# Optimization experiments

Hardware: AMD Instinct MI355X
Metric: run time of the kernel (lower is better)

## Reference

```python
import jax, jax.numpy as jnp
import numpy as np

N = 50000          # nodes per node type
F = 256            # input feature dim
C = 256            # hidden_channels
H, D = 8, 32       # heads, head_dim (C = H*D)
E = 200000         # edges per edge type
OUT = 16           # out_channels
SRC = (0, 1, 0)    # edge type -> source node-type index (user,item)
DST = (1, 0, 0)    # edge type -> destination node-type index
LABELED = 1        # labeled_class = 'item'


def setup_inputs() -> dict:
    key = jax.random.key(0)
    ks = jax.random.split(key, 24)
    s = 0.06  # ~1/sqrt(256) init scale
    inp = {
        'x': jax.random.normal(ks[0], (2, N, F), jnp.float32),
        'edge_index': jax.random.randint(ks[1], (3, 2, E), 0, N, jnp.int64),
        'lin_w': jax.random.normal(ks[2], (2, F, C), jnp.float32) * s,
        'lin_b': jnp.zeros((2, C), jnp.float32),
        'k_w': jax.random.normal(ks[3], (2, C, C), jnp.float32) * s,
        'k_b': jnp.zeros((2, C), jnp.float32),
        'q_w': jax.random.normal(ks[4], (2, C, C), jnp.float32) * s,
        'q_b': jnp.zeros((2, C), jnp.float32),
        'v_w': jax.random.normal(ks[5], (2, C, C), jnp.float32) * s,
        'v_b': jnp.zeros((2, C), jnp.float32),
        'a_w': jax.random.normal(ks[6], (2, C, C), jnp.float32) * s,
        'a_b': jnp.zeros((2, C), jnp.float32),
        'skip': jnp.ones((2,), jnp.float32),
        'a_rel': jax.random.normal(ks[7], (3, H, D, D), jnp.float32) * (1.0 / np.sqrt(D)),
        'm_rel': jax.random.normal(ks[8], (3, H, D, D), jnp.float32) * (1.0 / np.sqrt(D)),
        'p_rel': jnp.ones((3, H), jnp.float32),
        'out_w': jax.random.normal(ks[9], (C, OUT), jnp.float32) * s,
        'out_b': jnp.zeros((OUT,), jnp.float32),
    }
    return inp


def _segment_softmax(alpha, idx, n):
    # alpha: [E, H], idx: [E] destination node ids
    amax = jax.ops.segment_max(alpha, idx, num_segments=n)
    amax = jnp.where(jnp.isfinite(amax), amax, 0.0)
    ex = jnp.exp(alpha - amax[idx])
    den = jax.ops.segment_sum(ex, idx, num_segments=n)
    return ex / (den[idx] + 1e-16)


def reference(x, edge_index, lin_w, lin_b, k_w, k_b, q_w, q_b, v_w, v_b,
              a_w, a_b, skip, a_rel, m_rel, p_rel, out_w, out_b):
    # per-node-type input Linear + ReLU
    h = jax.nn.relu(jnp.einsum('tnf,tfc->tnc', x, lin_w) + lin_b[:, None, :])

    def proj(w, b):
        return (jnp.einsum('tnc,tce->tne', h, w) + b[:, None, :]).reshape(2, N, H, D)

    k = proj(k_w, k_b)
    q = proj(q_w, q_b)
    v = proj(v_w, v_b)

    agg = jnp.zeros((2, N, H, D), h.dtype)
    for t in range(3):  # fixed small loop over edge types
        s, d = SRC[t], DST[t]
        src_idx, dst_idx = edge_index[t, 0], edge_index[t, 1]
        # relation-specific transforms of source keys / values
        k_rel = jnp.einsum('nhd,hde->nhe', k[s], a_rel[t])
        v_rel = jnp.einsum('nhd,hde->nhe', v[s], m_rel[t])
        # per-edge attention logits [E, H]
        alpha = (q[d][dst_idx] * k_rel[src_idx]).sum(-1) * p_rel[t] / (D ** 0.5)
        alpha = _segment_softmax(alpha, dst_idx, N)
        msg = v_rel[src_idx] * alpha[..., None]          # [E, H, D]
        agg = agg.at[d].add(jax.ops.segment_sum(msg, dst_idx, num_segments=N))

    o = agg.reshape(2, N, C)
    o = jnp.einsum('tnc,tce->tne', jax.nn.gelu(o, approximate=False), a_w) + a_b[:, None, :]
    beta = jax.nn.sigmoid(skip)[:, None, None]
    o = beta * o + (1.0 - beta) * h                      # skip connection (in == out dims)

    return o[LABELED] @ out_w + out_b                    # logits for labeled_class='item'
```

## Files before the change

kernel.cpp:

```cpp
#include <hip/hip_runtime.h>
#include <hip/hip_bf16.h>

using u16 = unsigned short;
using u32 = unsigned int;

#define NNODES 50000
#define NEDGE  200000
#define DEGCAP 64
#define NT     3125

__device__ __forceinline__ float blo2f(u32 u) { u32 v = u << 16; float f; __builtin_memcpy(&f, &v, 4); return f; }
__device__ __forceinline__ float bhi2f(u32 u) { u32 v = u & 0xffff0000u; float f; __builtin_memcpy(&f, &v, 4); return f; }
__device__ __forceinline__ u16 f2b(float f) {
  __hip_bfloat16 h = __float2bfloat16(f);
  u16 r; __builtin_memcpy(&r, &h, 2); return r;
}
__device__ __forceinline__ float gelu_exact(float x) {
  return 0.5f * x * (1.f + erff(x * 0.70710678118654752f));
}

__device__ __forceinline__ void gload16(const void* gp, void* lp) {
  __builtin_amdgcn_global_load_lds(
      (__attribute__((address_space(1))) u32*)(const_cast<void*>(gp)),
      (__attribute__((address_space(3))) u32*)lp, 16, 0, 0);
}

#define WAIT_VM(N) asm volatile("s_waitcnt vmcnt(" #N ")" ::: "memory")

typedef __bf16 bh8 __attribute__((ext_vector_type(8)));
typedef float f32x4 __attribute__((ext_vector_type(4)));

struct GArg { const u16* A; const u16* B; const float* bias; u16* C; };

__device__ __forceinline__ void stage_blk_bf16(const u16* At, u16* buf, int wave, int lane) {
#pragma unroll
  for (int i = 0; i < 2; ++i) {
    const int row = wave * 4 + i * 2 + (lane >> 5);
    const int c   = (lane & 31) ^ (row & 7);
    gload16(At + (size_t)row * 256 + c * 8, buf + wave * 1024 + i * 512 + lane * 8);
  }
}

__device__ __forceinline__ void stage_blk_f32(const float* At, float* buf, int wave, int lane) {
#pragma unroll
  for (int i = 0; i < 4; ++i) {
    const int row = wave * 4 + i;
    const int c   = lane ^ (row & 7);
    gload16(At + (size_t)row * 256 + c * 4, buf + row * 256 + lane * 4);
  }
}

template <int MODE, bool F32A>
__launch_bounds__(256, 2)
__global__ void gemm_v10(GArg g0, GArg g1, GArg g2)
{
  GArg ga = (blockIdx.z == 0) ? g0 : ((blockIdx.z == 1) ? g1 : g2);
  const int tid  = threadIdx.x;
  const int lane = tid & 63;
  const int wave = tid >> 6;
  const int lr = lane & 15;
  const int lq = lane >> 4;
  const int colbase = wave * 64;

  constexpr int TW = F32A ? 8192 : 4096;
  __shared__ alignas(16) u16 lds[3][TW];
  __shared__ alignas(16) u16 pat[4][1152];
  u16* wl = &pat[wave][0];

  bh8 B[4][8];
#pragma unroll
  for (int s = 0; s < 4; ++s) {
    const u16* bp = ga.B + (size_t)(colbase + s * 16 + lr) * 256 + lq * 8;
#pragma unroll
    for (int ks = 0; ks < 8; ++ks) B[s][ks] = *(const bh8*)(bp + ks * 32);
  }
  float bias[4];
#pragma unroll
  for (int s = 0; s < 4; ++s) bias[s] = ga.bias[colbase + s * 16 + lr];

  int foffL[8], foffH[8];
#pragma unroll
  for (int ks = 0; ks < 8; ++ks) {
    if (F32A) {
      foffL[ks] = lr * 256 + (((ks * 8 + lq * 2)     ^ (lr & 7)) << 2);
      foffH[ks] = lr * 256 + (((ks * 8 + lq * 2 + 1) ^ (lr & 7)) << 2);
    } else {
      foffL[ks] = lr * 256 + (((ks * 4 + lq) ^ (lr & 7)) * 8);
    }
  }

  const int t0 = blockIdx.x;
  const int ts = gridDim.x;

  if (F32A) stage_blk_f32((const float*)ga.A + (size_t)t0 * 4096, (float*)&lds[0][0], wave, lane);
  else      stage_blk_bf16(ga.A + (size_t)t0 * 4096, &lds[0][0], wave, lane);
  if (t0 + ts < NT) {
    if (F32A) stage_blk_f32((const float*)ga.A + (size_t)(t0 + ts) * 4096, (float*)&lds[1][0], wave, lane);
    else      stage_blk_bf16(ga.A + (size_t)(t0 + ts) * 4096, &lds[1][0], wave, lane);
  }

  int it = 0, rb = 0;
  for (int t = t0; t < NT; t += ts, ++it) {
    const bool p1 = (t + ts < NT), p2 = (t + 2 * ts < NT);
    if (p2) {
      const int rn = (rb + 2 >= 3) ? rb - 1 : rb + 2;
      if (F32A) stage_blk_f32((const float*)ga.A + (size_t)(t + 2 * ts) * 4096, (float*)&lds[rn][0], wave, lane);
      else      stage_blk_bf16(ga.A + (size_t)(t + 2 * ts) * 4096, &lds[rn][0], wave, lane);
    }
    if (!p1)            { WAIT_VM(0); }
    else if (!p2)       { if (F32A) { WAIT_VM(6); }  else { WAIT_VM(4); } }
    else if (it >= 2)   { if (F32A) { WAIT_VM(12); } else { WAIT_VM(8); } }
    else                { if (F32A) { WAIT_VM(8); }  else { WAIT_VM(4); } }
    __builtin_amdgcn_s_barrier();

    bh8 ab[8];
    if (F32A) {
      const float* fbuf = (const float*)&lds[rb][0];
#pragma unroll
      for (int ks = 0; ks < 8; ++ks) {
        const f32x4 lo = *(const f32x4*)(fbuf + foffL[ks]);
        const f32x4 hi = *(const f32x4*)(fbuf + foffH[ks]);
#pragma unroll
        for (int j = 0; j < 4; ++j) { ab[ks][j] = (__bf16)lo[j]; ab[ks][j + 4] = (__bf16)hi[j]; }
      }
    } else {
      const u16* buf = &lds[rb][0];
#pragma unroll
      for (int ks = 0; ks < 8; ++ks) ab[ks] = *(const bh8*)(buf + foffL[ks]);
    }

    f32x4 acc[4];
#pragma unroll
    for (int s = 0; s < 4; ++s) acc[s] = (f32x4){0.f, 0.f, 0.f, 0.f};
#pragma unroll
    for (int ks = 0; ks < 8; ++ks) {
#pragma unroll
      for (int s = 0; s < 4; ++s)
        acc[s] = __builtin_amdgcn_mfma_f32_16x16x32_bf16(ab[ks], B[s][ks], acc[s], 0, 0, 0);
    }

#pragma unroll
    for (int s = 0; s < 4; ++s) {
#pragma unroll
      for (int r = 0; r < 4; ++r) {
        float v = acc[s][r] + bias[s];
        if (MODE == 0) v = fmaxf(v, 0.f);
        wl[(lq * 4 + r) * 72 + s * 16 + lr] = f2b(v);
      }
    }
#pragma unroll
    for (int j = 0; j < 2; ++j) {
      const int row = (lane >> 3) + j * 8;
      const int seg = lane & 7;
      const uint4 pv = *(const uint4*)(wl + row * 72 + seg * 8);
      *(uint4*)(ga.C + ((size_t)t * 16 + row) * 256 + colbase + seg * 8) = pv;
    }
    __builtin_amdgcn_s_barrier();
    rb = (rb + 1 == 3) ? 0 : rb + 1;
  }
}

__global__ void prep_w_k(const float* __restrict__ lin_w, const float* __restrict__ q_w,
                         const float* __restrict__ a_w, const float* __restrict__ k_w,
                         const float* __restrict__ v_w, const float* __restrict__ k_b,
                         const float* __restrict__ v_b, const float* __restrict__ a_rel,
                         const float* __restrict__ m_rel, const float* __restrict__ out_w,
                         const float* __restrict__ a_b, const float* __restrict__ out_b,
                         const float* __restrict__ skipv,
                         u16* __restrict__ lin0T, u16* __restrict__ lin1T,
                         u16* __restrict__ qT,
                         u16* __restrict__ kfT, u16* __restrict__ vfT,
                         u16* __restrict__ WcT, float* __restrict__ bfin,
                         float* __restrict__ bkf, float* __restrict__ bvf,
                         int* __restrict__ cnt)
{
  const int tid = blockIdx.x * 256 + threadIdx.x;
  const int nn = tid >> 8, kk = tid & 255;
  switch (blockIdx.y) {
    case 0: lin0T[tid] = f2b(lin_w[kk * 256 + nn]); break;
    case 1: lin1T[tid] = f2b(lin_w[65536 + kk * 256 + nn]); break;
    case 2: qT[tid] = f2b(q_w[65536 + kk * 256 + nn]); break;
    case 3: {
      const int h = nn >> 5, e = nn & 31;
      float s = 0.f;
      for (int d = 0; d < 32; ++d) s += k_w[kk * 256 + h * 32 + d] * a_rel[(h * 32 + d) * 32 + e];
      kfT[tid] = f2b(s);
      if (kk == 0) {
        float sb = 0.f;
        for (int d = 0; d < 32; ++d) sb += k_b[h * 32 + d] * a_rel[(h * 32 + d) * 32 + e];
        bkf[nn] = sb;
      }
      break;
    }
    case 4: {
      const int h = nn >> 5, e = nn & 31;
      float s = 0.f;
      for (int d = 0; d < 32; ++d) s += v_w[kk * 256 + h * 32 + d] * m_rel[(h * 32 + d) * 32 + e];
      vfT[tid] = f2b(s);
      if (kk == 0) {
        float sb = 0.f;
        for (int d = 0; d < 32; ++d) sb += v_b[h * 32 + d] * m_rel[(h * 32 + d) * 32 + e];
        bvf[nn] = sb;
      }
      break;
    }
    case 5: {
      const float beta = 1.f / (1.f + __expf(-skipv[1]));
      if (tid < 8192) {
        const int j = tid & 15;
        const int k = tid >> 4;
        float s;
        if (k < 256) {
          float acc = 0.f;
          for (int d = 0; d < 256; ++d)
            acc += a_w[65536 + k * 256 + d] * out_w[d * 16 + j];
          s = beta * acc;
        } else {
          s = (1.f - beta) * out_w[(k - 256) * 16 + j];
        }
        WcT[j * 512 + k] = f2b(s);
      }
      if (tid < 16) {
        float acc = 0.f;
        for (int c = 0; c < 256; ++c) acc += a_b[256 + c] * out_w[c * 16 + tid];
        bfin[tid] = beta * acc + out_b[tid];
      }
      break;
    }
    default:
      if (tid < NNODES) cnt[tid] = 0;
      break;
  }
}

__global__ void scatter_k(const int* __restrict__ ei, int* __restrict__ cnt, int* __restrict__ srcl) {
  const int e = blockIdx.x * 256 + threadIdx.x;
  if (e >= NEDGE) return;
  const int src = ei[e];
  const int dst = ei[NEDGE + e];
  if ((unsigned)dst >= NNODES || (unsigned)src >= NNODES) return;
  const int pos = atomicAdd(&cnt[dst], 1);
  if (pos < DEGCAP) srcl[(size_t)dst * DEGCAP + pos] = src;
}

__global__ void edge_agg_k(const u16* __restrict__ qb, const u16* __restrict__ krel,
                           const u16* __restrict__ vrel, const int* __restrict__ cnt,
                           const int* __restrict__ srcl, const float* __restrict__ prel,
                           u16* __restrict__ g)
{
  const int node = (blockIdx.x * blockDim.x + threadIdx.x) >> 6;
  if (node >= NNODES) return;
  const int lane = threadIdx.x & 63;
  const int hh = lane >> 3;
  const int off = hh * 32 + (lane & 7) * 4;
  const float scale = prel[hh] * 0.17677669529663687f;
  const uint2 qv = *(const uint2*)(qb + (size_t)node * 256 + off);
  const float q0 = blo2f(qv.x) * scale, q1 = bhi2f(qv.x) * scale;
  const float q2 = blo2f(qv.y) * scale, q3 = bhi2f(qv.y) * scale;
  int dg = cnt[node]; if (dg > DEGCAP) dg = DEGCAP;
  const int mysrc = srcl[(size_t)node * DEGCAP + lane];

  float den = 0.f, a0 = 0.f, a1 = 0.f, a2 = 0.f, a3 = 0.f;
  uint2 kv = {0, 0}, vv = {0, 0};
  if (dg > 0) {
    const int s0 = __shfl(mysrc, 0);
    kv = *(const uint2*)(krel + (size_t)s0 * 256 + off);
    vv = *(const uint2*)(vrel + (size_t)s0 * 256 + off);
  }
  for (int i = 0; i < dg; ++i) {
    uint2 kn = kv, vn = vv;
    if (i + 1 < dg) {
      const int sn = __shfl(mysrc, i + 1);
      kn = *(const uint2*)(krel + (size_t)sn * 256 + off);
      vn = *(const uint2*)(vrel + (size_t)sn * 256 + off);
    }
    float p = q0 * blo2f(kv.x) + q1 * bhi2f(kv.x) + q2 * blo2f(kv.y) + q3 * bhi2f(kv.y);
    p += __shfl_xor(p, 1);
    p += __shfl_xor(p, 2);
    p += __shfl_xor(p, 4);
    const float ex = __expf(p);
    den += ex;
    a0 += ex * blo2f(vv.x); a1 += ex * bhi2f(vv.x);
    a2 += ex * blo2f(vv.y); a3 += ex * bhi2f(vv.y);
    kv = kn; vv = vn;
  }
  float r0 = 0.f, r1 = 0.f, r2 = 0.f, r3 = 0.f;
  if (dg > 0) {
    const float inv = 1.f / den;
    r0 = gelu_exact(a0 * inv); r1 = gelu_exact(a1 * inv);
    r2 = gelu_exact(a2 * inv); r3 = gelu_exact(a3 * inv);
  }
  uint2 gv;
  gv.x = (u32)f2b(r0) | ((u32)f2b(r1) << 16);
  gv.y = (u32)f2b(r2) | ((u32)f2b(r3) << 16);
  *(uint2*)(g + (size_t)node * 256 + off) = gv;
}

__launch_bounds__(256, 3)
__global__ void final_v10(const u16* __restrict__ g, const u16* __restrict__ h1,
                          const u16* __restrict__ WcT, const float* __restrict__ bfin,
                          float* __restrict__ out)
{
  const int tid = threadIdx.x;
  const int lane = tid & 63;
  const int wave = tid >> 6;
  const int lr = lane & 15;
  const int lq = lane >> 4;

  __shared__ alignas(16) u16 lds[3][8192];
  __shared__ float red[4][256];

  bh8 B[4];
  {
    const u16* bp = WcT + (size_t)lr * 512 + wave * 128 + lq * 8;
#pragma unroll
    for (int ks = 0; ks < 4; ++ks) B[ks] = *(const bh8*)(bp + ks * 32);
  }
  const float bv = bfin[tid & 15];

  int foff[4];
#pragma unroll
  for (int ks = 0; ks < 4; ++ks)
    foff[ks] = wave * 2048 + lr * 128 + (((ks * 4 + lq) ^ (lr & 7)) * 8);

  const u16* srcq = (wave < 2) ? g + wave * 128 : h1 + (wave - 2) * 128;

  const int t0 = blockIdx.x;
  const int ts = gridDim.x;

#define FSTAGE(T, RB)                                                          \
  {                                                                            \
    _Pragma("unroll")                                                          \
    for (int i = 0; i < 4; ++i) {                                              \
      const int row = i * 4 + (lane >> 4);                                     \
      const int c   = (lane & 15) ^ (row & 7);                                 \
      gload16(srcq + (size_t)(T) * 4096 + row * 256 + c * 8,                   \
              &lds[RB][wave * 2048 + i * 512 + lane * 8]);                     \
    }                                                                          \
  }

  FSTAGE(t0, 0);
  if (t0 + ts < NT) FSTAGE(t0 + ts, 1);

  int it = 0, rb = 0;
  for (int t = t0; t < NT; t += ts, ++it) {
    const bool p1 = (t + ts < NT), p2 = (t + 2 * ts < NT);
    if (p2) {
      const int rn = (rb + 2 >= 3) ? rb - 1 : rb + 2;
      FSTAGE(t + 2 * ts, rn);
    }
    if (!p1)          { WAIT_VM(0); }
    else if (!p2)     { WAIT_VM(4); }
    else if (it >= 2) { WAIT_VM(10); }
    else              { WAIT_VM(8); }
    __builtin_amdgcn_s_barrier();

    f32x4 acc = {0.f, 0.f, 0.f, 0.f};
    const u16* buf = &lds[rb][0];
#pragma unroll
    for (int ks = 0; ks < 4; ++ks)
      acc = __builtin_amdgcn_mfma_f32_16x16x32_bf16(*(const bh8*)(buf + foff[ks]), B[ks], acc, 0, 0, 0);

#pragma unroll
    for (int r = 0; r < 4; ++r) red[wave][(lq * 4 + r) * 16 + lr] = acc[r];
    asm volatile("s_waitcnt lgkmcnt(0)" ::: "memory");
    __builtin_amdgcn_s_barrier();

    const float s = red[0][tid] + red[1][tid] + red[2][tid] + red[3][tid] + bv;
    out[(size_t)t * 256 + tid] = s;
    __builtin_amdgcn_s_barrier();
    rb = (rb + 1 == 3) ? 0 : rb + 1;
  }
#undef FSTAGE
}

extern "C" void kernel_launch(void* const* d_in, const int* in_sizes, int n_in,
                              void* d_out, int out_size, void* d_ws, size_t ws_size,
                              hipStream_t stream)
{
  const float* x     = (const float*)d_in[0];
  const int*   ei    = (const int*)d_in[1];
  const float* lin_w = (const float*)d_in[2];
  const float* lin_b = (const float*)d_in[3];
  const float* k_w   = (const float*)d_in[4];
  const float* k_b   = (const float*)d_in[5];
  const float* q_w   = (const float*)d_in[6];
  const float* q_b   = (const float*)d_in[7];
  const float* v_w   = (const float*)d_in[8];
  const float* v_b   = (const float*)d_in[9];
  const float* a_w   = (const float*)d_in[10];
  const float* a_b   = (const float*)d_in[11];
  const float* skipv = (const float*)d_in[12];
  const float* a_rel = (const float*)d_in[13];
  const float* m_rel = (const float*)d_in[14];
  const float* p_rel = (const float*)d_in[15];
  const float* out_w = (const float*)d_in[16];
  const float* out_b = (const float*)d_in[17];
  char* ws = (char*)d_ws;

  u16*  h0    = (u16*)(ws + 0);
  u16*  h1    = (u16*)(ws + 25600000);
  u16*  qb    = (u16*)(ws + 51200000);
  u16*  krel  = (u16*)(ws + 76800000);
  u16*  vrel  = (u16*)(ws + 102400000);
  u16*  gbuf  = (u16*)(ws + 128000000);
  char* W     = ws + 153600000;
  u16*  lin0T = (u16*)(W + 0);
  u16*  lin1T = (u16*)(W + 131072);
  u16*  qT    = (u16*)(W + 2 * 131072);
  u16*  kfT   = (u16*)(W + 3 * 131072);
  u16*  vfT   = (u16*)(W + 4 * 131072);
  u16*  WcT   = (u16*)(W + 5 * 131072);
  float* bfin = (float*)(W + 5 * 131072 + 16384);
  float* bkf  = (float*)(W + 5 * 131072 + 17408);
  float* bvf  = (float*)(W + 5 * 131072 + 18432);
  int*  cnt   = (int*)(W + 5 * 131072 + 19456);
  int*  srcl  = (int*)(W + 5 * 131072 + 19456 + 200000);

  prep_w_k<<<dim3(256, 7), 256, 0, stream>>>(lin_w, q_w, a_w, k_w, v_w, k_b, v_b,
                                             a_rel, m_rel, out_w, a_b, out_b, skipv,
                                             lin0T, lin1T, qT, kfT, vfT, WcT, bfin,
                                             bkf, bvf, cnt);
  scatter_k<<<(NEDGE + 255) / 256, 256, 0, stream>>>(ei, cnt, srcl);

  {
    GArg a0{(const u16*)x, lin0T, lin_b, h0};
    GArg a1{(const u16*)(x + (size_t)NNODES * 256), lin1T, lin_b + 256, h1};
    gemm_v10<0, true><<<dim3(256, 1, 2), 256, 0, stream>>>(a0, a1, a0);
  }
  {
    GArg a0{h1, qT, q_b + 256, qb};
    GArg a1{h0, kfT, bkf, krel};
    GArg a2{h0, vfT, bvf, vrel};
    gemm_v10<1, false><<<dim3(170, 1, 3), 256, 0, stream>>>(a0, a1, a2);
  }
  edge_agg_k<<<12500, 256, 0, stream>>>(qb, krel, vrel, cnt, srcl, p_rel, gbuf);
  final_v10<<<768, 256, 0, stream>>>(gbuf, h1, WcT, bfin, (float*)d_out);
}
```

Baseline: 322.4 us.

## Split GEMM columns across blocks and use register-staged double buffering

```diff
diff --git a/kernel.cpp b/kernel.cpp
--- a/kernel.cpp
+++ b/kernel.cpp
@@ -32,27 +32,9 @@
 
 struct GArg { const u16* A; const u16* B; const float* bias; u16* C; };
 
-__device__ __forceinline__ void stage_blk_bf16(const u16* At, u16* buf, int wave, int lane) {
-#pragma unroll
-  for (int i = 0; i < 2; ++i) {
-    const int row = wave * 4 + i * 2 + (lane >> 5);
-    const int c   = (lane & 31) ^ (row & 7);
-    gload16(At + (size_t)row * 256 + c * 8, buf + wave * 1024 + i * 512 + lane * 8);
-  }
-}
-
-__device__ __forceinline__ void stage_blk_f32(const float* At, float* buf, int wave, int lane) {
-#pragma unroll
-  for (int i = 0; i < 4; ++i) {
-    const int row = wave * 4 + i;
-    const int c   = lane ^ (row & 7);
-    gload16(At + (size_t)row * 256 + c * 4, buf + row * 256 + lane * 4);
-  }
-}
-
 template <int MODE, bool F32A>
-__launch_bounds__(256, 2)
-__global__ void gemm_v10(GArg g0, GArg g1, GArg g2)
+__launch_bounds__(256, 3)
+__global__ void gemm_v14(GArg g0, GArg g1, GArg g2)
 {
   GArg ga = (blockIdx.z == 0) ? g0 : ((blockIdx.z == 1) ? g1 : g2);
   const int tid  = threadIdx.x;
@@ -60,23 +42,23 @@
   const int wave = tid >> 6;
   const int lr = lane & 15;
   const int lq = lane >> 4;
-  const int colbase = wave * 64;
+  const int colbase = blockIdx.y * 128 + wave * 32;
 
   constexpr int TW = F32A ? 8192 : 4096;
-  __shared__ alignas(16) u16 lds[3][TW];
-  __shared__ alignas(16) u16 pat[4][1152];
+  __shared__ alignas(16) u16 lds[2][TW];
+  __shared__ alignas(16) u16 pat[4][640];
   u16* wl = &pat[wave][0];
 
-  bh8 B[4][8];
-#pragma unroll
-  for (int s = 0; s < 4; ++s) {
+  bh8 B[2][8];
+#pragma unroll
+  for (int s = 0; s < 2; ++s) {
     const u16* bp = ga.B + (size_t)(colbase + s * 16 + lr) * 256 + lq * 8;
 #pragma unroll
     for (int ks = 0; ks < 8; ++ks) B[s][ks] = *(const bh8*)(bp + ks * 32);
   }
-  float bias[4];
-#pragma unroll
-  for (int s = 0; s < 4; ++s) bias[s] = ga.bias[colbase + s * 16 + lr];
+  float bias[2];
+#pragma unroll
+  for (int s = 0; s < 2; ++s) bias[s] = ga.bias[colbase + s * 16 + lr];
 
   int foffL[8], foffH[8];
 #pragma unroll
@@ -92,30 +74,54 @@
   const int t0 = blockIdx.x;
   const int ts = gridDim.x;
 
-  if (F32A) stage_blk_f32((const float*)ga.A + (size_t)t0 * 4096, (float*)&lds[0][0], wave, lane);
-  else      stage_blk_bf16(ga.A + (size_t)t0 * 4096, &lds[0][0], wave, lane);
-  if (t0 + ts < NT) {
-    if (F32A) stage_blk_f32((const float*)ga.A + (size_t)(t0 + ts) * 4096, (float*)&lds[1][0], wave, lane);
-    else      stage_blk_bf16(ga.A + (size_t)(t0 + ts) * 4096, &lds[1][0], wave, lane);
-  }
-
-  int it = 0, rb = 0;
-  for (int t = t0; t < NT; t += ts, ++it) {
-    const bool p1 = (t + ts < NT), p2 = (t + 2 * ts < NT);
-    if (p2) {
-      const int rn = (rb + 2 >= 3) ? rb - 1 : rb + 2;
-      if (F32A) stage_blk_f32((const float*)ga.A + (size_t)(t + 2 * ts) * 4096, (float*)&lds[rn][0], wave, lane);
-      else      stage_blk_bf16(ga.A + (size_t)(t + 2 * ts) * 4096, &lds[rn][0], wave, lane);
-    }
-    if (!p1)            { WAIT_VM(0); }
-    else if (!p2)       { if (F32A) { WAIT_VM(6); }  else { WAIT_VM(4); } }
-    else if (it >= 2)   { if (F32A) { WAIT_VM(12); } else { WAIT_VM(8); } }
-    else                { if (F32A) { WAIT_VM(8); }  else { WAIT_VM(4); } }
-    __builtin_amdgcn_s_barrier();
+  f32x4 rf[4];
+  uint4  rb2[2];
+
+#define LOADR(T)                                                               \
+  if (F32A) {                                                                  \
+    const float* ap = (const float*)ga.A + ((size_t)(T) * 16 + wave * 4) * 256 \
+                      + lane * 4;                                              \
+    _Pragma("unroll")                                                          \
+    for (int i = 0; i < 4; ++i) rf[i] = *(const f32x4*)(ap + i * 256);         \
+  } else {                                                                     \
+    _Pragma("unroll")                                                          \
+    for (int i = 0; i < 2; ++i) {                                              \
+      const int row = wave * 4 + i * 2 + (lane >> 5);                          \
+      rb2[i] = *(const uint4*)(ga.A + ((size_t)(T) * 16 + row) * 256           \
+                               + (lane & 31) * 8);                             \
+    }                                                                          \
+  }
+
+#define WRITER(P)                                                              \
+  if (F32A) {                                                                  \
+    float* bp = (float*)&lds[P][0];                                            \
+    _Pragma("unroll")                                                          \
+    for (int i = 0; i < 4; ++i) {                                              \
+      const int row = wave * 4 + i;                                            \
+      *(f32x4*)(bp + row * 256 + ((lane ^ (row & 7)) << 2)) = rf[i];           \
+    }                                                                          \
+  } else {                                                                     \
+    _Pragma("unroll")                                                          \
+    for (int i = 0; i < 2; ++i) {                                              \
+      const int row = wave * 4 + i * 2 + (lane >> 5);                          \
+      *(uint4*)(&lds[P][row * 256 + (((lane & 31) ^ (row & 7)) * 8)]) = rb2[i];\
+    }                                                                          \
+  }
+
+  LOADR(t0);
+  WAIT_VM(0);
+  WRITER(0);
+  asm volatile("s_waitcnt lgkmcnt(0)" ::: "memory");
+  __builtin_amdgcn_s_barrier();
+
+  int p = 0;
+  for (int t = t0; t < NT; t += ts) {
+    const bool pn = (t + ts < NT);
+    if (pn) LOADR(t + ts);
 
     bh8 ab[8];
     if (F32A) {
-      const float* fbuf = (const float*)&lds[rb][0];
+      const float* fbuf = (const float*)&lds[p][0];
 #pragma unroll
       for (int ks = 0; ks < 8; ++ks) {
         const f32x4 lo = *(const f32x4*)(fbuf + foffL[ks]);
@@ -124,40 +130,46 @@
         for (int j = 0; j < 4; ++j) { ab[ks][j] = (__bf16)lo[j]; ab[ks][j + 4] = (__bf16)hi[j]; }
       }
     } else {
-      const u16* buf = &lds[rb][0];
+      const u16* buf = &lds[p][0];
 #pragma unroll
       for (int ks = 0; ks < 8; ++ks) ab[ks] = *(const bh8*)(buf + foffL[ks]);
     }
 
-    f32x4 acc[4];
-#pragma unroll
-    for (int s = 0; s < 4; ++s) acc[s] = (f32x4){0.f, 0.f, 0.f, 0.f};
+    f32x4 acc[2];
+#pragma unroll
+    for (int s = 0; s < 2; ++s) acc[s] = (f32x4){0.f, 0.f, 0.f, 0.f};
 #pragma unroll
     for (int ks = 0; ks < 8; ++ks) {
 #pragma unroll
-      for (int s = 0; s < 4; ++s)
+      for (int s = 0; s < 2; ++s)
         acc[s] = __builtin_amdgcn_mfma_f32_16x16x32_bf16(ab[ks], B[s][ks], acc[s], 0, 0, 0);
     }
 
 #pragma unroll
-    for (int s = 0; s < 4; ++s) {
+    for (int s = 0; s < 2; ++s) {
 #pragma unroll
       for (int r = 0; r < 4; ++r) {
         float v = acc[s][r] + bias[s];
         if (MODE == 0) v = fmaxf(v, 0.f);
-        wl[(lq * 4 + r) * 72 + s * 16 + lr] = f2b(v);
-      }
-    }
-#pragma unroll
-    for (int j = 0; j < 2; ++j) {
-      const int row = (lane >> 3) + j * 8;
-      const int seg = lane & 7;
-      const uint4 pv = *(const uint4*)(wl + row * 72 + seg * 8);
+        wl[(lq * 4 + r) * 40 + s * 16 + lr] = f2b(v);
+      }
+    }
+    {
+      const int row = lane >> 2, seg = lane & 3;
+      const uint4 pv = *(const uint4*)(wl + row * 40 + seg * 8);
       *(uint4*)(ga.C + ((size_t)t * 16 + row) * 256 + colbase + seg * 8) = pv;
     }
+
+    if (pn) {
+      WAIT_VM(1);
+      WRITER(p ^ 1);
+    }
+    asm volatile("s_waitcnt lgkmcnt(0)" ::: "memory");
     __builtin_amdgcn_s_barrier();
-    rb = (rb + 1 == 3) ? 0 : rb + 1;
-  }
+    p ^= 1;
+  }
+#undef LOADR
+#undef WRITER
 }
 
 __global__ void prep_w_k(const float* __restrict__ lin_w, const float* __restrict__ q_w,
@@ -426,13 +438,13 @@
   {
     GArg a0{(const u16*)x, lin0T, lin_b, h0};
     GArg a1{(const u16*)(x + (size_t)NNODES * 256), lin1T, lin_b + 256, h1};
-    gemm_v10<0, true><<<dim3(256, 1, 2), 256, 0, stream>>>(a0, a1, a0);
+    gemm_v14<0, true><<<dim3(192, 2, 2), 256, 0, stream>>>(a0, a1, a0);
   }
   {
     GArg a0{h1, qT, q_b + 256, qb};
     GArg a1{h0, kfT, bkf, krel};
     GArg a2{h0, vfT, bvf, vrel};
-    gemm_v10<1, false><<<dim3(170, 1, 3), 256, 0, stream>>>(a0, a1, a2);
+    gemm_v14<1, false><<<dim3(128, 2, 3), 256, 0, stream>>>(a0, a1, a2);
   }
   edge_agg_k<<<12500, 256, 0, stream>>>(qb, krel, vrel, cnt, srcl, p_rel, gbuf);
   final_v10<<<768, 256, 0, stream>>>(gbuf, h1, WcT, bfin, (float*)d_out);
```

Result: slower. 341.7 us (+6.0%).

## Fuse edge aggregation with final output projection into one persistent kernel

Applied to the files above, without the earlier changes.

```diff
diff --git a/kernel.cpp b/kernel.cpp
--- a/kernel.cpp
+++ b/kernel.cpp
@@ -14,6 +14,9 @@
 __device__ __forceinline__ u16 f2b(float f) {
   __hip_bfloat16 h = __float2bfloat16(f);
   u16 r; __builtin_memcpy(&r, &h, 2); return r;
+}
+__device__ __forceinline__ u32 pack2(float a, float b) {
+  return (u32)f2b(a) | ((u32)f2b(b) << 16);
 }
 __device__ __forceinline__ float gelu_exact(float x) {
   return 0.5f * x * (1.f + erff(x * 0.70710678118654752f));
@@ -170,7 +173,7 @@
                          u16* __restrict__ lin0T, u16* __restrict__ lin1T,
                          u16* __restrict__ qT,
                          u16* __restrict__ kfT, u16* __restrict__ vfT,
-                         u16* __restrict__ WcT, float* __restrict__ bfin,
+                         u16* __restrict__ Wpk, float* __restrict__ bfin,
                          float* __restrict__ bkf, float* __restrict__ bvf,
                          int* __restrict__ cnt)
 {
@@ -218,7 +221,7 @@
         } else {
           s = (1.f - beta) * out_w[(k - 256) * 16 + j];
         }
-        WcT[j * 512 + k] = f2b(s);
+        Wpk[k * 16 + j] = f2b(s);
       }
       if (tid < 16) {
         float acc = 0.f;
@@ -243,135 +246,105 @@
   if (pos < DEGCAP) srcl[(size_t)dst * DEGCAP + pos] = src;
 }
 
-__global__ void edge_agg_k(const u16* __restrict__ qb, const u16* __restrict__ krel,
-                           const u16* __restrict__ vrel, const int* __restrict__ cnt,
-                           const int* __restrict__ srcl, const float* __restrict__ prel,
-                           u16* __restrict__ g)
+__launch_bounds__(256, 3)
+__global__ void edge_final_k(const u16* __restrict__ qb, const u16* __restrict__ krel,
+                             const u16* __restrict__ vrel, const int* __restrict__ cnt,
+                             const int* __restrict__ srcl, const float* __restrict__ prel,
+                             const u16* __restrict__ h1, const u16* __restrict__ Wpk,
+                             const float* __restrict__ bfin, float* __restrict__ out)
 {
-  const int node = (blockIdx.x * blockDim.x + threadIdx.x) >> 6;
-  if (node >= NNODES) return;
   const int lane = threadIdx.x & 63;
+  const int wave = threadIdx.x >> 6;
+  __shared__ alignas(8) u16 owl[4][512];
+  u16* wlds = &owl[wave][0];
+
   const int hh = lane >> 3;
   const int off = hh * 32 + (lane & 7) * 4;
   const float scale = prel[hh] * 0.17677669529663687f;
-  const uint2 qv = *(const uint2*)(qb + (size_t)node * 256 + off);
-  const float q0 = blo2f(qv.x) * scale, q1 = bhi2f(qv.x) * scale;
-  const float q2 = blo2f(qv.y) * scale, q3 = bhi2f(qv.y) * scale;
-  int dg = cnt[node]; if (dg > DEGCAP) dg = DEGCAP;
-  const int mysrc = srcl[(size_t)node * DEGCAP + lane];
-
-  float den = 0.f, a0 = 0.f, a1 = 0.f, a2 = 0.f, a3 = 0.f;
-  uint2 kv = {0, 0}, vv = {0, 0};
-  if (dg > 0) {
-    const int s0 = __shfl(mysrc, 0);
-    kv = *(const uint2*)(krel + (size_t)s0 * 256 + off);
-    vv = *(const uint2*)(vrel + (size_t)s0 * 256 + off);
-  }
-  for (int i = 0; i < dg; ++i) {
-    uint2 kn = kv, vn = vv;
-    if (i + 1 < dg) {
-      const int sn = __shfl(mysrc, i + 1);
-      kn = *(const uint2*)(krel + (size_t)sn * 256 + off);
-      vn = *(const uint2*)(vrel + (size_t)sn * 256 + off);
-    }
-    float p = q0 * blo2f(kv.x) + q1 * bhi2f(kv.x) + q2 * blo2f(kv.y) + q3 * bhi2f(kv.y);
-    p += __shfl_xor(p, 1);
-    p += __shfl_xor(p, 2);
-    p += __shfl_xor(p, 4);
-    const float ex = __expf(p);
-    den += ex;
-    a0 += ex * blo2f(vv.x); a1 += ex * bhi2f(vv.x);
-    a2 += ex * blo2f(vv.y); a3 += ex * bhi2f(vv.y);
-    kv = kn; vv = vn;
-  }
-  float r0 = 0.f, r1 = 0.f, r2 = 0.f, r3 = 0.f;
-  if (dg > 0) {
-    const float inv = 1.f / den;
-    r0 = gelu_exact(a0 * inv); r1 = gelu_exact(a1 * inv);
-    r2 = gelu_exact(a2 * inv); r3 = gelu_exact(a3 * inv);
-  }
-  uint2 gv;
-  gv.x = (u32)f2b(r0) | ((u32)f2b(r1) << 16);
-  gv.y = (u32)f2b(r2) | ((u32)f2b(r3) << 16);
-  *(uint2*)(g + (size_t)node * 256 + off) = gv;
-}
-
-__launch_bounds__(256, 3)
-__global__ void final_v10(const u16* __restrict__ g, const u16* __restrict__ h1,
-                          const u16* __restrict__ WcT, const float* __restrict__ bfin,
-                          float* __restrict__ out)
-{
-  const int tid = threadIdx.x;
-  const int lane = tid & 63;
-  const int wave = tid >> 6;
-  const int lr = lane & 15;
-  const int lq = lane >> 4;
-
-  __shared__ alignas(16) u16 lds[3][8192];
-  __shared__ float red[4][256];
-
-  bh8 B[4];
-  {
-    const u16* bp = WcT + (size_t)lr * 512 + wave * 128 + lq * 8;
-#pragma unroll
-    for (int ks = 0; ks < 4; ++ks) B[ks] = *(const bh8*)(bp + ks * 32);
-  }
-  const float bv = bfin[tid & 15];
-
-  int foff[4];
-#pragma unroll
-  for (int ks = 0; ks < 4; ++ks)
-    foff[ks] = wave * 2048 + lr * 128 + (((ks * 4 + lq) ^ (lr & 7)) * 8);
-
-  const u16* srcq = (wave < 2) ? g + wave * 128 : h1 + (wave - 2) * 128;
-
-  const int t0 = blockIdx.x;
-  const int ts = gridDim.x;
-
-#define FSTAGE(T, RB)                                                          \
-  {                                                                            \
-    _Pragma("unroll")                                                          \
-    for (int i = 0; i < 4; ++i) {                                              \
-      const int row = i * 4 + (lane >> 4);                                     \
-      const int c   = (lane & 15) ^ (row & 7);                                 \
-      gload16(srcq + (size_t)(T) * 4096 + row * 256 + c * 8,                   \
-              &lds[RB][wave * 2048 + i * 512 + lane * 8]);                     \
-    }                                                                          \
-  }
-
-  FSTAGE(t0, 0);
-  if (t0 + ts < NT) FSTAGE(t0 + ts, 1);
-
-  int it = 0, rb = 0;
-  for (int t = t0; t < NT; t += ts, ++it) {
-    const bool p1 = (t + ts < NT), p2 = (t + 2 * ts < NT);
-    if (p2) {
-      const int rn = (rb + 2 >= 3) ? rb - 1 : rb + 2;
-      FSTAGE(t + 2 * ts, rn);
-    }
-    if (!p1)          { WAIT_VM(0); }
-    else if (!p2)     { WAIT_VM(4); }
-    else if (it >= 2) { WAIT_VM(10); }
-    else              { WAIT_VM(8); }
-    __builtin_amdgcn_s_barrier();
-
-    f32x4 acc = {0.f, 0.f, 0.f, 0.f};
-    const u16* buf = &lds[rb][0];
-#pragma unroll
-    for (int ks = 0; ks < 4; ++ks)
-      acc = __builtin_amdgcn_mfma_f32_16x16x32_bf16(*(const bh8*)(buf + foff[ks]), B[ks], acc, 0, 0, 0);
-
-#pragma unroll
-    for (int r = 0; r < 4; ++r) red[wave][(lq * 4 + r) * 16 + lr] = acc[r];
+
+  const int jg = lane >> 4;
+  const int cbase = (lane & 15) * 32;
+  uint2 W[32];
+#pragma unroll
+  for (int i = 0; i < 32; ++i)
+    W[i] = *(const uint2*)(Wpk + (size_t)(cbase + i) * 16 + jg * 4);
+  float bj[4];
+#pragma unroll
+  for (int r = 0; r < 4; ++r) bj[r] = bfin[jg * 4 + r];
+
+  const int wid0 = blockIdx.x * 4 + wave;
+  const int wstride = gridDim.x * 4;
+
+  for (int node = wid0; node < NNODES; node += wstride) {
+    const uint2 qv = *(const uint2*)(qb + (size_t)node * 256 + off);
+    const float q0 = blo2f(qv.x) * scale, q1 = bhi2f(qv.x) * scale;
+    const float q2 = blo2f(qv.y) * scale, q3 = bhi2f(qv.y) * scale;
+    int dg = cnt[node]; if (dg > DEGCAP) dg = DEGCAP;
+    const int mysrc = srcl[(size_t)node * DEGCAP + lane];
+
+    float den = 0.f, a0 = 0.f, a1 = 0.f, a2 = 0.f, a3 = 0.f;
+    uint2 kv = {0, 0}, vv = {0, 0};
+    if (dg > 0) {
+      const int s0 = __shfl(mysrc, 0);
+      kv = *(const uint2*)(krel + (size_t)s0 * 256 + off);
+      vv = *(const uint2*)(vrel + (size_t)s0 * 256 + off);
+    }
+    for (int i = 0; i < dg; ++i) {
+      uint2 kn = kv, vn = vv;
+      if (i + 1 < dg) {
+        const int sn = __shfl(mysrc, i + 1);
+        kn = *(const uint2*)(krel + (size_t)sn * 256 + off);
+        vn = *(const uint2*)(vrel + (size_t)sn * 256 + off);
+      }
+      float p = q0 * blo2f(kv.x) + q1 * bhi2f(kv.x) + q2 * blo2f(kv.y) + q3 * bhi2f(kv.y);
+      p += __shfl_xor(p, 1);
+      p += __shfl_xor(p, 2);
+      p += __shfl_xor(p, 4);
+      const float ex = __expf(p);
+      den += ex;
+      a0 += ex * blo2f(vv.x); a1 += ex * bhi2f(vv.x);
+      a2 += ex * blo2f(vv.y); a3 += ex * bhi2f(vv.y);
+      kv = kn; vv = vn;
+    }
+    float r0 = 0.f, r1 = 0.f, r2 = 0.f, r3 = 0.f;
+    if (dg > 0) {
+      const float inv = 1.f / den;
+      r0 = gelu_exact(a0 * inv); r1 = gelu_exact(a1 * inv);
+      r2 = gelu_exact(a2 * inv); r3 = gelu_exact(a3 * inv);
+    }
+
+    const uint2 hv = *(const uint2*)(h1 + (size_t)node * 256 + off);
+    uint2 ov; ov.x = pack2(r0, r1); ov.y = pack2(r2, r3);
+    *(uint2*)(wlds + off)       = ov;
+    *(uint2*)(wlds + 256 + off) = hv;
     asm volatile("s_waitcnt lgkmcnt(0)" ::: "memory");
-    __builtin_amdgcn_s_barrier();
-
-    const float s = red[0][tid] + red[1][tid] + red[2][tid] + red[3][tid] + bv;
-    out[(size_t)t * 256 + tid] = s;
-    __builtin_amdgcn_s_barrier();
-    rb = (rb + 1 == 3) ? 0 : rb + 1;
-  }
-#undef FSTAGE
+
+    uint4 cv[4];
+#pragma unroll
+    for (int i = 0; i < 4; ++i) cv[i] = *(const uint4*)(wlds + cbase + i * 8);
+
+    float p0 = 0.f, p1 = 0.f, p2 = 0.f, p3 = 0.f;
+#pragma unroll
+    for (int rr = 0; rr < 32; ++rr) {
+      const u32 w32 = (rr & 4) ? ((rr & 2) ? cv[rr >> 3].w : cv[rr >> 3].z)
+                               : ((rr & 2) ? cv[rr >> 3].y : cv[rr >> 3].x);
+      const float oc = (rr & 1) ? bhi2f(w32) : blo2f(w32);
+      const uint2 wv = W[rr];
+      p0 += oc * blo2f(wv.x); p1 += oc * bhi2f(wv.x);
+      p2 += oc * blo2f(wv.y); p3 += oc * bhi2f(wv.y);
+    }
+#pragma unroll
+    for (int m = 1; m <= 8; m <<= 1) {
+      p0 += __shfl_xor(p0, m); p1 += __shfl_xor(p1, m);
+      p2 += __shfl_xor(p2, m); p3 += __shfl_xor(p3, m);
+    }
+    if ((lane & 15) == 0) {
+      float* op = out + (size_t)node * 16 + jg * 4;
+      op[0] = p0 + bj[0]; op[1] = p1 + bj[1];
+      op[2] = p2 + bj[2]; op[3] = p3 + bj[3];
+    }
+    asm volatile("s_waitcnt lgkmcnt(0)" ::: "memory");
+  }
 }
 
 extern "C" void kernel_launch(void* const* d_in, const int* in_sizes, int n_in,
@@ -403,14 +376,13 @@
   u16*  qb    = (u16*)(ws + 51200000);
   u16*  krel  = (u16*)(ws + 76800000);
   u16*  vrel  = (u16*)(ws + 102400000);
-  u16*  gbuf  = (u16*)(ws + 128000000);
   char* W     = ws + 153600000;
   u16*  lin0T = (u16*)(W + 0);
   u16*  lin1T = (u16*)(W + 131072);
   u16*  qT    = (u16*)(W + 2 * 131072);
   u16*  kfT   = (u16*)(W + 3 * 131072);
   u16*  vfT   = (u16*)(W + 4 * 131072);
-  u16*  WcT   = (u16*)(W + 5 * 131072);
+  u16*  Wpk   = (u16*)(W + 5 * 131072);
   float* bfin = (float*)(W + 5 * 131072 + 16384);
   float* bkf  = (float*)(W + 5 * 131072 + 17408);
   float* bvf  = (float*)(W + 5 * 131072 + 18432);
@@ -419,7 +391,7 @@
 
   prep_w_k<<<dim3(256, 7), 256, 0, stream>>>(lin_w, q_w, a_w, k_w, v_w, k_b, v_b,
                                              a_rel, m_rel, out_w, a_b, out_b, skipv,
-                                             lin0T, lin1T, qT, kfT, vfT, WcT, bfin,
+                                             lin0T, lin1T, qT, kfT, vfT, Wpk, bfin,
                                              bkf, bvf, cnt);
   scatter_k<<<(NEDGE + 255) / 256, 256, 0, stream>>>(ei, cnt, srcl);
 
@@ -434,6 +406,6 @@
     GArg a2{h0, vfT, bvf, vrel};
     gemm_v10<1, false><<<dim3(170, 1, 3), 256, 0, stream>>>(a0, a1, a2);
   }
-  edge_agg_k<<<12500, 256, 0, stream>>>(qb, krel, vrel, cnt, srcl, p_rel, gbuf);
-  final_v10<<<768, 256, 0, stream>>>(gbuf, h1, WcT, bfin, (float*)d_out);
-}
+  edge_final_k<<<1024, 256, 0, stream>>>(qb, krel, vrel, cnt, srcl, p_rel,
+                                         h1, Wpk, bfin, (float*)d_out);
+}
```

Result: slower. 448.7 us (+39.2%).
